# Performance work log

Measured on AMD Instinct MI355X. Metric: run time of the kernel, lower is better.

Reference implementation:

```python
import jax, jax.numpy as jnp
import numpy as np

D = 1024      # input_dim
H = 16        # num_heads
DH = D // H   # head dim
HID = 4 * D   # SwiGLU hidden
WIN = 128
B, S = 2, 1024


def setup_inputs() -> dict:
    key = jax.random.key(0)
    ks = jax.random.split(key, 16)
    n = lambda k, sh, sc=0.02: jax.random.normal(k, sh, dtype=jnp.float32) * sc
    inp = {
        "fusion": jax.random.normal(ks[0], (B, S, D), dtype=jnp.float32),
        "visual": jax.random.normal(ks[1], (B, S, D), dtype=jnp.float32),
        "text": jax.random.normal(ks[2], (B, S, D), dtype=jnp.float32),
        "audio": jax.random.normal(ks[3], (B, S, D), dtype=jnp.float32),
        "ln1_g": jnp.ones((D,), jnp.float32),
        "ln1_b": jnp.zeros((D,), jnp.float32),
        "Wqkv": n(ks[4], (D, 3 * D)),
        "bqkv": jnp.zeros((3 * D,), jnp.float32),
        "Wo": n(ks[5], (D, D)),
        "bo": jnp.zeros((D,), jnp.float32),
        "ln2_g": jnp.ones((D,), jnp.float32),
        "ln2_b": jnp.zeros((D,), jnp.float32),
        "W1": n(ks[6], (D, HID)),
        "b1": jnp.zeros((HID,), jnp.float32),
        "W2": n(ks[7], (D, HID)),
        "b2": jnp.zeros((HID,), jnp.float32),
        "W3": n(ks[8], (HID, D)),
        "b3": jnp.zeros((D,), jnp.float32),
    }
    return inp


def _layernorm(x, g, b, eps=1e-5):
    mu = jnp.mean(x, axis=-1, keepdims=True)
    var = jnp.var(x, axis=-1, keepdims=True)
    return (x - mu) * jax.lax.rsqrt(var + eps) * g + b


def _block(x, ln1_g, ln1_b, Wqkv, bqkv, Wo, bo, ln2_g, ln2_b, W1, b1, W2, b2, W3, b3):
    # x: [N, S, D] (N = 4*B streams stacked)
    N, S_, _ = x.shape
    h = _layernorm(x, ln1_g, ln1_b)
    qkv = h @ Wqkv + bqkv                              # [N, S, 3D]
    q, k, v = jnp.split(qkv, 3, axis=-1)
    to_heads = lambda t: t.reshape(N, S_, H, DH).transpose(0, 2, 1, 3)  # [N,H,S,DH]
    q, k, v = to_heads(q), to_heads(k), to_heads(v)
    scores = jnp.einsum("nhqd,nhkd->nhqk", q, k) / np.sqrt(DH)
    i = jnp.arange(S_)
    band = jnp.abs(i[:, None] - i[None, :]) <= WIN     # [S, S] local window mask
    scores = jnp.where(band, scores, -jnp.inf)
    probs = jax.nn.softmax(scores, axis=-1)
    ctx = jnp.einsum("nhqk,nhkd->nhqd", probs, v)      # [N,H,S,DH]
    ctx = ctx.transpose(0, 2, 1, 3).reshape(N, S_, D)
    x = x + (ctx @ Wo + bo)
    h2 = _layernorm(x, ln2_g, ln2_b)
    ffn = (jax.nn.silu(h2 @ W1 + b1) * (h2 @ W2 + b2)) @ W3 + b3
    return x + ffn


def reference(fusion, visual, text, audio, ln1_g, ln1_b, Wqkv, bqkv, Wo, bo,
              ln2_g, ln2_b, W1, b1, W2, b2, W3, b3):
    # Same layer applied to each modality -> stack and run once.
    x = jnp.concatenate([fusion, visual, text, audio], axis=0)  # [4B, S, D]
    y = _block(x, ln1_g, ln1_b, Wqkv, bqkv, Wo, bo, ln2_g, ln2_b,
               W1, b1, W2, b2, W3, b3)
    f, vi, t, a = jnp.split(y, 4, axis=0)
    return (f, vi, t, a)
```

## Files before the change

kernel.cpp:

```cpp
#include <hip/hip_runtime.h>

#define S_LEN  1024
#define DMODEL 1024
#define NHEAD  16
#define DHEAD  64
#define MROWS  8192
#define HIDDIM 4096
#define WINR   128

typedef __attribute__((ext_vector_type(8))) short bf16x8;
typedef __attribute__((ext_vector_type(4))) float f32x4;

__device__ __forceinline__ float bf2f(unsigned short u){ return __uint_as_float(((unsigned)u) << 16); }
__device__ __forceinline__ unsigned short f2bf(float f){
  unsigned u = __float_as_uint(f);
  u += 0x7FFFu + ((u >> 16) & 1u);
  return (unsigned short)(u >> 16);
}

__device__ __forceinline__ void gload_lds16(const unsigned short* g, unsigned short* l){
  __builtin_amdgcn_global_load_lds((const __attribute__((address_space(1))) unsigned int*)g,
                                   (__attribute__((address_space(3))) unsigned int*)l, 16, 0, 0);
}

__global__ __launch_bounds__(256) void transpose_w(const float* __restrict__ in,
                                                   unsigned short* __restrict__ out,
                                                   int R, int C){
  __shared__ float tile[32][33];
  const int c0 = blockIdx.x * 32;
  const int r0 = blockIdx.y * 32;
  const int tx = threadIdx.x & 31;
  const int ty = threadIdx.x >> 5;
  #pragma unroll
  for (int i = 0; i < 32; i += 8)
    tile[ty + i][tx] = in[(size_t)(r0 + ty + i) * C + c0 + tx];
  __syncthreads();
  #pragma unroll
  for (int i = 0; i < 32; i += 8)
    out[(size_t)(c0 + ty + i) * R + r0 + tx] = f2bf(tile[tx][ty + i]);
}

__global__ __launch_bounds__(256) void ln_kernel(const float* __restrict__ s0, const float* __restrict__ s1,
                                                 const float* __restrict__ s2, const float* __restrict__ s3,
                                                 const float* __restrict__ g, const float* __restrict__ b,
                                                 unsigned short* __restrict__ out){
  const int row = blockIdx.x;
  const int t = threadIdx.x;
  const float* src = (row < 2048) ? s0 : (row < 4096) ? s1 : (row < 6144) ? s2 : s3;
  const float* x = src + (size_t)(row & 2047) * DMODEL;
  float4 v = *(const float4*)&x[t * 4];
  float sum  = v.x + v.y + v.z + v.w;
  float ssum = v.x*v.x + v.y*v.y + v.z*v.z + v.w*v.w;
  #pragma unroll
  for (int o = 32; o > 0; o >>= 1){
    sum  += __shfl_down(sum, o);
    ssum += __shfl_down(ssum, o);
  }
  __shared__ float red[8];
  if ((t & 63) == 0){ red[t >> 6] = sum; red[4 + (t >> 6)] = ssum; }
  __syncthreads();
  sum  = red[0] + red[1] + red[2] + red[3];
  ssum = red[4] + red[5] + red[6] + red[7];
  const float mu  = sum * (1.f / DMODEL);
  const float var = ssum * (1.f / DMODEL) - mu * mu;
  const float rs  = rsqrtf(var + 1e-5f);
  float4 gg = *(const float4*)&g[t * 4];
  float4 bb = *(const float4*)&b[t * 4];
  ushort4 o;
  o.x = f2bf((v.x - mu) * rs * gg.x + bb.x);
  o.y = f2bf((v.y - mu) * rs * gg.y + bb.y);
  o.z = f2bf((v.z - mu) * rs * gg.z + bb.z);
  o.w = f2bf((v.w - mu) * rs * gg.w + bb.w);
  *(ushort4*)&out[(size_t)row * DMODEL + t * 4] = o;
}

__global__ __launch_bounds__(256) void attn_kernel(const unsigned short* __restrict__ qh,
                                                   const unsigned short* __restrict__ kh,
                                                   const unsigned short* __restrict__ vt,
                                                   unsigned short* __restrict__ ctx){
  __shared__ unsigned short Ks[64 * 64];
  __shared__ unsigned short Vs[64 * 64];
  __shared__ unsigned short Ps[4][16 * 64];
  const int bx = blockIdx.x;
  const int qt = bx & 15, hd = (bx >> 4) & 15, n = bx >> 8;
  const int q0 = qt * 64;
  const int tid = threadIdx.x, lane = tid & 63, w = tid >> 6;
  const int hi = lane >> 4, lo = lane & 15;
  const size_t headoff = (size_t)(n * NHEAD + hd) * S_LEN * DHEAD;
  const unsigned short* kb = kh + headoff;
  const unsigned short* vb = vt + headoff;

  const int qg = q0 + w * 16 + lo;
  bf16x8 bq0 = *(const bf16x8*)(qh + headoff + (size_t)qg * DHEAD + hi * 8);
  bf16x8 bq1 = *(const bf16x8*)(qh + headoff + (size_t)qg * DHEAD + 32 + hi * 8);

  f32x4 oa[4];
  const f32x4 zero = {0.f, 0.f, 0.f, 0.f};
  #pragma unroll
  for (int dj = 0; dj < 4; dj++) oa[dj] = zero;
  float m = -20.f, lsum = 0.f;

  int t_first = q0 - WINR; if (t_first < 0) t_first = 0;
  int t_last  = q0 + 63 + WINR; if (t_last > S_LEN - 1) t_last = S_LEN - 1;

  const int sk = ((lane & 7) ^ (lane >> 3)) * 8;
  const int px = (lo & 7) * 8;

  for (int tb = t_first; tb <= t_last; tb += 64){
    __syncthreads();
    #pragma unroll
    for (int p = 0; p < 2; p++){
      const int r = w * 16 + p * 8 + (lane >> 3);
      gload_lds16(kb + (size_t)(tb + r) * DHEAD + sk, Ks + (w * 16 + p * 8) * 64);
      gload_lds16(vb + (size_t)r * S_LEN + tb + sk, Vs + (w * 16 + p * 8) * 64);
    }
    __syncthreads();

    f32x4 sc[4];
    #pragma unroll
    for (int j = 0; j < 4; j++){
      const int row = j * 16 + lo;
      bf16x8 ak0 = *(const bf16x8*)&Ks[row * 64 + ((hi * 8) ^ px)];
      bf16x8 ak1 = *(const bf16x8*)&Ks[row * 64 + ((32 + hi * 8) ^ px)];
      sc[j] = __builtin_amdgcn_mfma_f32_16x16x32_bf16(ak0, bq0, zero, 0, 0, 0);
      sc[j] = __builtin_amdgcn_mfma_f32_16x16x32_bf16(ak1, bq1, sc[j], 0, 0, 0);
    }

    float mloc = -1e30f;
    #pragma unroll
    for (int j = 0; j < 4; j++)
      #pragma unroll
      for (int r = 0; r < 4; r++){
        const int key = tb + j * 16 + hi * 4 + r;
        float s = sc[j][r] * 0.125f;
        s = ((unsigned)(key - qg + WINR) <= 2u * WINR) ? s : -1e9f;
        sc[j][r] = s;
        mloc = fmaxf(mloc, s);
      }
    mloc = fmaxf(mloc, __shfl_xor(mloc, 16));
    mloc = fmaxf(mloc, __shfl_xor(mloc, 32));
    const float nm = fmaxf(m, mloc);
    const float scale = __expf(m - nm);
    m = nm;
    float psum = 0.f;
    #pragma unroll
    for (int j = 0; j < 4; j++){
      float p0 = __expf(sc[j][0] - nm), p1 = __expf(sc[j][1] - nm);
      float p2 = __expf(sc[j][2] - nm), p3 = __expf(sc[j][3] - nm);
      psum += (p0 + p1) + (p2 + p3);
      ushort4 pw = { f2bf(p0), f2bf(p1), f2bf(p2), f2bf(p3) };
      *(ushort4*)&Ps[w][lo * 64 + ((hi * 4 + 16 * j) ^ px)] = pw;
    }
    psum += __shfl_xor(psum, 16);
    psum += __shfl_xor(psum, 32);
    lsum = lsum * scale + psum;

    float scr[4];
    #pragma unroll
    for (int r = 0; r < 4; r++) scr[r] = __shfl(scale, (lane & 48) + hi * 4 + r);
    #pragma unroll
    for (int dj = 0; dj < 4; dj++)
      #pragma unroll
      for (int r = 0; r < 4; r++) oa[dj][r] *= scr[r];

    bf16x8 pa0 = *(const bf16x8*)&Ps[w][lo * 64 + ((hi * 8) ^ px)];
    bf16x8 pa1 = *(const bf16x8*)&Ps[w][lo * 64 + ((32 + hi * 8) ^ px)];
    #pragma unroll
    for (int dj = 0; dj < 4; dj++){
      const int dr = dj * 16 + lo;
      bf16x8 bv0 = *(const bf16x8*)&Vs[dr * 64 + ((hi * 8) ^ px)];
      bf16x8 bv1 = *(const bf16x8*)&Vs[dr * 64 + ((32 + hi * 8) ^ px)];
      oa[dj] = __builtin_amdgcn_mfma_f32_16x16x32_bf16(pa0, bv0, oa[dj], 0, 0, 0);
      oa[dj] = __builtin_amdgcn_mfma_f32_16x16x32_bf16(pa1, bv1, oa[dj], 0, 0, 0);
    }
  }

  const float inv = 1.f / lsum;
  float invr[4];
  #pragma unroll
  for (int r = 0; r < 4; r++) invr[r] = __shfl(inv, (lane & 48) + hi * 4 + r);
  #pragma unroll
  for (int dj = 0; dj < 4; dj++)
    #pragma unroll
    for (int r = 0; r < 4; r++){
      const int srow = q0 + w * 16 + hi * 4 + r;
      ctx[((size_t)(n * S_LEN + srow)) * DMODEL + hd * DHEAD + dj * 16 + lo] =
          f2bf(oa[dj][r] * invr[r]);
    }
}

struct GemmP {
  const unsigned short* A;
  const unsigned short* Bt;
  int K;
  int N;
  const float* bias;
  const float* r0; const float* r1; const float* r2; const float* r3;
  unsigned short* oq; unsigned short* ok; unsigned short* ov;
  float* of;
};

template<int MODE>
__global__ __launch_bounds__(256, 2) void gemm_bn128(GemmP p){
  __shared__ unsigned short ldsA[2][128 * 64];
  __shared__ unsigned short ldsB[2][128 * 64];
  const int tid  = threadIdx.x;
  const int lane = tid & 63;
  const int w    = tid >> 6;
  const int lo   = lane & 15, hi = lane >> 4;
  const int l3   = lane >> 3;
  const int sk   = ((lane & 7) ^ l3) * 8;
  const int wm   = (w >> 1) * 64;
  const int wn   = (w & 1) * 64;
  const int K    = p.K;

  const int nwg = gridDim.x;
  const int cpx = nwg >> 3;
  const int bsw = ((int)blockIdx.x & 7) * cpx + ((int)blockIdx.x >> 3);
  const int ntn = p.N >> 7;
  const int m0  = (bsw / ntn) * 128;
  const int n0  = (bsw % ntn) * 128;

  f32x4 acc[4][4];
  const f32x4 zero = {0.f, 0.f, 0.f, 0.f};
  #pragma unroll
  for (int i = 0; i < 4; i++)
    #pragma unroll
    for (int j = 0; j < 4; j++) acc[i][j] = zero;

  auto STAGE = [&](int T){
    const int cur = T & 1;
    const int kb  = T * 64;
    #pragma unroll
    for (int c = 0; c < 4; c++){
      const int r0 = w * 32 + c * 8;
      gload_lds16(p.A + (size_t)(m0 + r0 + l3) * K + kb + sk, &ldsA[cur][r0 * 64]);
    }
    #pragma unroll
    for (int c = 0; c < 4; c++){
      const int r0 = w * 32 + c * 8;
      gload_lds16(p.Bt + (size_t)(n0 + r0 + l3) * K + kb + sk, &ldsB[cur][r0 * 64]);
    }
  };

  STAGE(0);

  const int NT = K >> 6;
  for (int T = 0; T < NT; T++){
    const int cur = T & 1;
    if (T + 1 < NT){
      STAGE(T + 1);
      asm volatile("s_waitcnt vmcnt(8)" ::: "memory");
    } else {
      asm volatile("s_waitcnt vmcnt(0)" ::: "memory");
    }
    __builtin_amdgcn_sched_barrier(0);
    __builtin_amdgcn_s_barrier();
    const unsigned short* As_ = ldsA[cur];
    const unsigned short* Bs_ = ldsB[cur];
    #pragma unroll
    for (int kk = 0; kk < 2; kk++){
      bf16x8 af[4], bfr[4];
      #pragma unroll
      for (int i = 0; i < 4; i++){
        const int R = wm + i * 16 + lo;
        af[i] = *(const bf16x8*)&As_[R * 64 + (((kk * 4 + hi) ^ (R & 7)) * 8)];
      }
      #pragma unroll
      for (int j = 0; j < 4; j++){
        const int R = wn + j * 16 + lo;
        bfr[j] = *(const bf16x8*)&Bs_[R * 64 + (((kk * 4 + hi) ^ (R & 7)) * 8)];
      }
      #pragma unroll
      for (int i = 0; i < 4; i++)
        #pragma unroll
        for (int j = 0; j < 4; j++)
          acc[i][j] = __builtin_amdgcn_mfma_f32_16x16x32_bf16(bfr[j], af[i], acc[i][j], 0, 0, 0);
    }
    __builtin_amdgcn_s_barrier();
  }

  if constexpr (MODE == 1 || MODE == 4){
    const float* rs = p.r0;
    if constexpr (MODE == 1){
      const int rblk = m0 + wm;
      rs = (rblk < 2048) ? p.r0 : (rblk < 4096) ? p.r1 : (rblk < 6144) ? p.r2 : p.r3;
    }
    #pragma unroll
    for (int i = 0; i < 4; i++){
      const int row = m0 + wm + i * 16 + lo;
      #pragma unroll
      for (int j = 0; j < 4; j++){
        const int cb = n0 + wn + j * 16 + hi * 4;
        float4 b4 = *(const float4*)&p.bias[cb];
        float4 r4;
        if constexpr (MODE == 1) r4 = *(const float4*)&rs[(size_t)(row & 2047) * DMODEL + cb];
        else                     r4 = *(const float4*)&rs[(size_t)row * DMODEL + cb];
        float4 v;
        v.x = acc[i][j][0] + b4.x + r4.x;
        v.y = acc[i][j][1] + b4.y + r4.y;
        v.z = acc[i][j][2] + b4.z + r4.z;
        v.w = acc[i][j][3] + b4.w + r4.w;
        *(float4*)&p.of[(size_t)row * DMODEL + cb] = v;
      }
    }
  } else {
    __syncthreads();
    unsigned short* sl = &ldsA[0][0] + w * 4096;
    const int nseq = (m0 + wm) >> 10;
    const int sof  = (m0 + wm) & 1023;
    const bool isV = (n0 >> 10) == 2;
    if (!isV){
      #pragma unroll
      for (int i = 0; i < 4; i++){
        const int row = i * 16 + lo;
        #pragma unroll
        for (int j = 0; j < 4; j++){
          const int c  = j * 16 + hi * 4;
          const int cb = n0 + wn + c;
          float4 b4 = *(const float4*)&p.bias[cb];
          ushort4 o = { f2bf(acc[i][j][0] + b4.x), f2bf(acc[i][j][1] + b4.y),
                        f2bf(acc[i][j][2] + b4.z), f2bf(acc[i][j][3] + b4.w) };
          *(ushort4*)&sl[row * 64 + (((c >> 3) ^ (row & 7)) * 8) + (c & 7)] = o;
        }
      }
      asm volatile("s_waitcnt lgkmcnt(0)" ::: "memory");
      __builtin_amdgcn_sched_barrier(0);
      #pragma unroll
      for (int rep = 0; rep < 8; rep++){
        const int row = rep * 8 + l3;
        const int ch  = lane & 7;
        bf16x8 val = *(const bf16x8*)&sl[row * 64 + ((ch ^ (row & 7)) * 8)];
        const int cg = n0 + wn + ch * 8;
        const int hh = (cg & 1023) >> 6, d0 = cg & 63;
        unsigned short* dst = (cg >> 10) ? p.ok : p.oq;
        *(bf16x8*)&dst[((size_t)((nseq * NHEAD + hh) * S_LEN) + sof + row) * DHEAD + d0] = val;
      }
    } else {
      #pragma unroll
      for (int i = 0; i < 4; i++){
        const int s = i * 16 + lo;
        #pragma unroll
        for (int j = 0; j < 4; j++){
          const int cb = n0 + wn + j * 16 + hi * 4;
          float4 b4 = *(const float4*)&p.bias[cb];
          #pragma unroll
          for (int r = 0; r < 4; r++){
            const int d = j * 16 + hi * 4 + r;
            const float bv = (r == 0) ? b4.x : (r == 1) ? b4.y : (r == 2) ? b4.z : b4.w;
            sl[d * 64 + (((s >> 3) ^ (d & 7)) * 8) + (s & 7)] = f2bf(acc[i][j][r] + bv);
          }
        }
      }
      asm volatile("s_waitcnt lgkmcnt(0)" ::: "memory");
      __builtin_amdgcn_sched_barrier(0);
      #pragma unroll
      for (int rep = 0; rep < 8; rep++){
        const int d  = rep * 8 + l3;
        const int ch = lane & 7;
        bf16x8 val = *(const bf16x8*)&sl[d * 64 + ((ch ^ (d & 7)) * 8)];
        const int cg = n0 + wn + d;
        const int hh = (cg & 1023) >> 6, dd = cg & 63;
        *(bf16x8*)&p.ov[((size_t)((nseq * NHEAD + hh) * DHEAD) + dd) * S_LEN + sof + ch * 8] = val;
      }
    }
  }
}

__global__ __launch_bounds__(256, 2) void gemm_ffn(const unsigned short* __restrict__ A,
                                                   const unsigned short* __restrict__ B1t,
                                                   const unsigned short* __restrict__ B2t,
                                                   const float* __restrict__ b1,
                                                   const float* __restrict__ b2,
                                                   unsigned short* __restrict__ out){
  __shared__ unsigned short ldsA[128 * 64];
  __shared__ unsigned short ldsB1[128 * 64];
  __shared__ unsigned short ldsB2[128 * 64];
  const int tid  = threadIdx.x;
  const int lane = tid & 63;
  const int w    = tid >> 6;
  const int lo   = lane & 15, hi = lane >> 4;
  const int l3   = lane >> 3;
  const int sk   = ((lane & 7) ^ l3) * 8;
  const int wm   = (w >> 1) * 64;
  const int wn   = (w & 1) * 64;

  const int nwg = gridDim.x;
  const int cpx = nwg >> 3;
  const int bsw = ((int)blockIdx.x & 7) * cpx + ((int)blockIdx.x >> 3);
  const int m0  = (bsw >> 5) * 128;
  const int n0  = (bsw & 31) * 128;

  f32x4 a1[4][4], a2[4][4];
  const f32x4 zero = {0.f, 0.f, 0.f, 0.f};
  #pragma unroll
  for (int i = 0; i < 4; i++)
    #pragma unroll
    for (int j = 0; j < 4; j++){ a1[i][j] = zero; a2[i][j] = zero; }

  const int NT = DMODEL >> 6;
  for (int T = 0; T < NT; T++){
    const int kb = T * 64;
    __syncthreads();
    #pragma unroll
    for (int c = 0; c < 4; c++){
      const int r0 = w * 32 + c * 8;
      gload_lds16(A   + (size_t)(m0 + r0 + l3) * DMODEL + kb + sk, &ldsA[r0 * 64]);
      gload_lds16(B1t + (size_t)(n0 + r0 + l3) * DMODEL + kb + sk, &ldsB1[r0 * 64]);
      gload_lds16(B2t + (size_t)(n0 + r0 + l3) * DMODEL + kb + sk, &ldsB2[r0 * 64]);
    }
    __syncthreads();

    #pragma unroll
    for (int kk = 0; kk < 2; kk++){
      bf16x8 af[4], bf1[4], bf2[4];
      #pragma unroll
      for (int i = 0; i < 4; i++){
        const int R = wm + i * 16 + lo;
        af[i] = *(const bf16x8*)&ldsA[R * 64 + (((kk * 4 + hi) ^ (R & 7)) * 8)];
      }
      #pragma unroll
      for (int j = 0; j < 4; j++){
        const int R = wn + j * 16 + lo;
        const int off = R * 64 + (((kk * 4 + hi) ^ (R & 7)) * 8);
        bf1[j] = *(const bf16x8*)&ldsB1[off];
        bf2[j] = *(const bf16x8*)&ldsB2[off];
      }
      #pragma unroll
      for (int i = 0; i < 4; i++)
        #pragma unroll
        for (int j = 0; j < 4; j++){
          a1[i][j] = __builtin_amdgcn_mfma_f32_16x16x32_bf16(bf1[j], af[i], a1[i][j], 0, 0, 0);
          a2[i][j] = __builtin_amdgcn_mfma_f32_16x16x32_bf16(bf2[j], af[i], a2[i][j], 0, 0, 0);
        }
    }
  }

  __syncthreads();
  unsigned short* sl = &ldsA[0] + w * 4096;
  #pragma unroll
  for (int i = 0; i < 4; i++){
    const int row = i * 16 + lo;
    #pragma unroll
    for (int j = 0; j < 4; j++){
      const int c  = j * 16 + hi * 4;
      const int cb = n0 + wn + c;
      float4 g1 = *(const float4*)&b1[cb];
      float4 g2 = *(const float4*)&b2[cb];
      float v1[4] = { a1[i][j][0] + g1.x, a1[i][j][1] + g1.y, a1[i][j][2] + g1.z, a1[i][j][3] + g1.w };
      float v2[4] = { a2[i][j][0] + g2.x, a2[i][j][1] + g2.y, a2[i][j][2] + g2.z, a2[i][j][3] + g2.w };
      ushort4 o;
      o.x = f2bf(v1[0] / (1.f + __expf(-v1[0])) * v2[0]);
      o.y = f2bf(v1[1] / (1.f + __expf(-v1[1])) * v2[1]);
      o.z = f2bf(v1[2] / (1.f + __expf(-v1[2])) * v2[2]);
      o.w = f2bf(v1[3] / (1.f + __expf(-v1[3])) * v2[3]);
      *(ushort4*)&sl[row * 64 + (((c >> 3) ^ (row & 7)) * 8) + (c & 7)] = o;
    }
  }
  asm volatile("s_waitcnt lgkmcnt(0)" ::: "memory");
  __builtin_amdgcn_sched_barrier(0);
  #pragma unroll
  for (int rep = 0; rep < 8; rep++){
    const int row = rep * 8 + l3;
    const int ch  = lane & 7;
    bf16x8 val = *(const bf16x8*)&sl[row * 64 + ((ch ^ (row & 7)) * 8)];
    *(bf16x8*)&out[(size_t)(m0 + wm + row) * HIDDIM + n0 + wn + ch * 8] = val;
  }
}

extern "C" void kernel_launch(void* const* d_in, const int* in_sizes, int n_in,
                              void* d_out, int out_size, void* d_ws, size_t ws_size,
                              hipStream_t stream){
  const float* fin  = (const float*)d_in[0];
  const float* vis  = (const float*)d_in[1];
  const float* txt  = (const float*)d_in[2];
  const float* aud  = (const float*)d_in[3];
  const float* ln1g = (const float*)d_in[4];
  const float* ln1b = (const float*)d_in[5];
  const float* Wqkv = (const float*)d_in[6];
  const float* bqkv = (const float*)d_in[7];
  const float* Wo   = (const float*)d_in[8];
  const float* bo   = (const float*)d_in[9];
  const float* ln2g = (const float*)d_in[10];
  const float* ln2b = (const float*)d_in[11];
  const float* W1   = (const float*)d_in[12];
  const float* b1   = (const float*)d_in[13];
  const float* W2   = (const float*)d_in[14];
  const float* b2   = (const float*)d_in[15];
  const float* W3   = (const float*)d_in[16];
  const float* b3   = (const float*)d_in[17];

  char* ws = (char*)d_ws;
  unsigned short* Wqkv_t = (unsigned short*)(ws + 0);
  unsigned short* Wo_t   = (unsigned short*)(ws + 6291456);
  unsigned short* W1t    = (unsigned short*)(ws + 8388608);
  unsigned short* W2t    = (unsigned short*)(ws + 16777216);
  unsigned short* W3t    = (unsigned short*)(ws + 25165824);
  unsigned short* h      = (unsigned short*)(ws + 33554432);
  unsigned short* qh     = (unsigned short*)(ws + 50331648);
  unsigned short* kh     = (unsigned short*)(ws + 67108864);
  unsigned short* vhT    = (unsigned short*)(ws + 83886080);
  unsigned short* ctx    = (unsigned short*)(ws + 100663296);
  float*          x1     = (float*)(ws + 117440512);
  unsigned short* t1     = qh;

  transpose_w<<<dim3(3072/32, 1024/32), 256, 0, stream>>>(Wqkv, Wqkv_t, 1024, 3072);
  transpose_w<<<dim3(1024/32, 1024/32), 256, 0, stream>>>(Wo,   Wo_t,   1024, 1024);
  transpose_w<<<dim3(4096/32, 1024/32), 256, 0, stream>>>(W1,   W1t,    1024, 4096);
  transpose_w<<<dim3(4096/32, 1024/32), 256, 0, stream>>>(W2,   W2t,    1024, 4096);
  transpose_w<<<dim3(1024/32, 4096/32), 256, 0, stream>>>(W3,   W3t,    4096, 1024);

  ln_kernel<<<MROWS, 256, 0, stream>>>(fin, vis, txt, aud, ln1g, ln1b, h);

  {
    GemmP p{};
    p.A = h; p.Bt = Wqkv_t; p.K = 1024; p.N = 3072; p.bias = bqkv;
    p.oq = qh; p.ok = kh; p.ov = vhT;
    gemm_bn128<0><<<1536, 256, 0, stream>>>(p);
  }

  attn_kernel<<<2048, 256, 0, stream>>>(qh, kh, vhT, ctx);

  {
    GemmP p{};
    p.A = ctx; p.Bt = Wo_t; p.K = 1024; p.N = 1024; p.bias = bo;
    p.r0 = fin; p.r1 = vis; p.r2 = txt; p.r3 = aud;
    p.of = x1;
    gemm_bn128<1><<<512, 256, 0, stream>>>(p);
  }

  ln_kernel<<<MROWS, 256, 0, stream>>>(x1, x1 + (size_t)2048 * 1024, x1 + (size_t)4096 * 1024,
                                       x1 + (size_t)6144 * 1024, ln2g, ln2b, h);

  gemm_ffn<<<2048, 256, 0, stream>>>(h, W1t, W2t, b1, b2, t1);

  {
    GemmP p{};
    p.A = t1; p.Bt = W3t; p.K = HIDDIM; p.N = 1024; p.bias = b3;
    p.r0 = x1;
    p.of = (float*)d_out;
    gemm_bn128<4><<<512, 256, 0, stream>>>(p);
  }

  (void)in_sizes; (void)n_in; (void)out_size; (void)ws_size;
}
```

Measured before the change: 389.1 us.

## Single-buffer LDS in projection GEMM and raise occupancy launch bounds

Replaces the double-buffered global-to-LDS prefetch pipeline in gemm_bn128 with a single LDS buffer loaded and consumed between two __syncthreads per K-tile. This halves the GEMM's LDS footprint, and launch bounds rise from 2 to 4 blocks per CU, so more workgroups can be resident to hide memory latency. gemm_ffn's launch bounds also rise from 2 to 3. The cost is that global loads no longer overlap MFMA work within a block, and the tighter register budget may cause spills with 64 accumulator floats per lane. The epilogue still indexes ldsA at w*4096, which now runs past ldsA into whatever LDS follows it.

New measurement: 699.0 us. 79.6% more time.

```diff
diff --git a/kernel.cpp b/kernel.cpp
--- a/kernel.cpp
+++ b/kernel.cpp
@@ -201,9 +201,9 @@
 };
 
 template<int MODE>
-__global__ __launch_bounds__(256, 2) void gemm_bn128(GemmP p){
-  __shared__ unsigned short ldsA[2][128 * 64];
-  __shared__ unsigned short ldsB[2][128 * 64];
+__global__ __launch_bounds__(256, 4) void gemm_bn128(GemmP p){
+  __shared__ unsigned short ldsA[128 * 64];
+  __shared__ unsigned short ldsB[128 * 64];
   const int tid  = threadIdx.x;
   const int lane = tid & 63;
   const int w    = tid >> 6;
@@ -228,48 +228,30 @@
     #pragma unroll
     for (int j = 0; j < 4; j++) acc[i][j] = zero;
 
-  auto STAGE = [&](int T){
-    const int cur = T & 1;
-    const int kb  = T * 64;
+  const int NT = K >> 6;
+  for (int T = 0; T < NT; T++){
+    const int kb = T * 64;
+    __syncthreads();
     #pragma unroll
     for (int c = 0; c < 4; c++){
       const int r0 = w * 32 + c * 8;
-      gload_lds16(p.A + (size_t)(m0 + r0 + l3) * K + kb + sk, &ldsA[cur][r0 * 64]);
-    }
-    #pragma unroll
-    for (int c = 0; c < 4; c++){
-      const int r0 = w * 32 + c * 8;
-      gload_lds16(p.Bt + (size_t)(n0 + r0 + l3) * K + kb + sk, &ldsB[cur][r0 * 64]);
-    }
-  };
-
-  STAGE(0);
-
-  const int NT = K >> 6;
-  for (int T = 0; T < NT; T++){
-    const int cur = T & 1;
-    if (T + 1 < NT){
-      STAGE(T + 1);
-      asm volatile("s_waitcnt vmcnt(8)" ::: "memory");
-    } else {
-      asm volatile("s_waitcnt vmcnt(0)" ::: "memory");
-    }
-    __builtin_amdgcn_sched_barrier(0);
-    __builtin_amdgcn_s_barrier();
-    const unsigned short* As_ = ldsA[cur];
-    const unsigned short* Bs_ = ldsB[cur];
+      gload_lds16(p.A  + (size_t)(m0 + r0 + l3) * K + kb + sk, &ldsA[r0 * 64]);
+      gload_lds16(p.Bt + (size_t)(n0 + r0 + l3) * K + kb + sk, &ldsB[r0 * 64]);
+    }
+    __syncthreads();
+
     #pragma unroll
     for (int kk = 0; kk < 2; kk++){
       bf16x8 af[4], bfr[4];
       #pragma unroll
       for (int i = 0; i < 4; i++){
         const int R = wm + i * 16 + lo;
-        af[i] = *(const bf16x8*)&As_[R * 64 + (((kk * 4 + hi) ^ (R & 7)) * 8)];
+        af[i] = *(const bf16x8*)&ldsA[R * 64 + (((kk * 4 + hi) ^ (R & 7)) * 8)];
       }
       #pragma unroll
       for (int j = 0; j < 4; j++){
         const int R = wn + j * 16 + lo;
-        bfr[j] = *(const bf16x8*)&Bs_[R * 64 + (((kk * 4 + hi) ^ (R & 7)) * 8)];
+        bfr[j] = *(const bf16x8*)&ldsB[R * 64 + (((kk * 4 + hi) ^ (R & 7)) * 8)];
       }
       #pragma unroll
       for (int i = 0; i < 4; i++)
@@ -277,7 +259,6 @@
         for (int j = 0; j < 4; j++)
           acc[i][j] = __builtin_amdgcn_mfma_f32_16x16x32_bf16(bfr[j], af[i], acc[i][j], 0, 0, 0);
     }
-    __builtin_amdgcn_s_barrier();
   }
 
   if constexpr (MODE == 1 || MODE == 4){
@@ -306,7 +287,7 @@
     }
   } else {
     __syncthreads();
-    unsigned short* sl = &ldsA[0][0] + w * 4096;
+    unsigned short* sl = &ldsA[0] + w * 4096;
     const int nseq = (m0 + wm) >> 10;
     const int sof  = (m0 + wm) & 1023;
     const bool isV = (n0 >> 10) == 2;
@@ -367,7 +348,7 @@
   }
 }
 
-__global__ __launch_bounds__(256, 2) void gemm_ffn(const unsigned short* __restrict__ A,
+__global__ __launch_bounds__(256, 3) void gemm_ffn(const unsigned short* __restrict__ A,
                                                    const unsigned short* __restrict__ B1t,
                                                    const unsigned short* __restrict__ B2t,
                                                    const float* __restrict__ b1,
```
